# Optimization experiments

Hardware: AMD Instinct MI355X
Metric: run time of the kernel (lower is better)

Reference implementation:

```python
import jax, jax.numpy as jnp
import numpy as np

# Camera / renderer constants from the original forward():
#   renderer.eye = get_points_from_angles(2.732, 0, 90); Renderer defaults.
DIST, ELEV, AZIM = 2.732, 0.0, 90.0
VIEW_ANGLE = 30.0          # neural_renderer Renderer default viewing angle (deg)
S = 256                    # image_size (Renderer default)
SIGMA = 3e-3               # softness of the differentiable edge test
EPS = 1e-12


def _normalize(v):
    return v / (jnp.linalg.norm(v) + EPS)


def _project(vertices):
    """look_at + perspective projection -> 2D NDC coords. vertices: [B,N,3]."""
    e = jnp.deg2rad(jnp.float32(ELEV))
    a = jnp.deg2rad(jnp.float32(AZIM))
    eye = jnp.array([DIST * jnp.cos(e) * jnp.sin(a),
                     DIST * jnp.sin(e),
                     -DIST * jnp.cos(e) * jnp.cos(a)], dtype=jnp.float32)
    at = jnp.zeros(3, jnp.float32)
    up = jnp.array([0.0, 1.0, 0.0], jnp.float32)
    zax = _normalize(at - eye)
    xax = _normalize(jnp.cross(up, zax))
    yax = jnp.cross(zax, xax)
    R = jnp.stack([xax, yax, zax])                 # [3,3], rows = camera axes
    v_cam = (vertices - eye) @ R.T                 # [B,N,3]
    w = jnp.tan(jnp.deg2rad(jnp.float32(VIEW_ANGLE)))
    z = jnp.maximum(v_cam[..., 2], 1e-2)           # guard behind-camera verts
    return v_cam[..., :2] / (z[..., None] * w)     # [B,N,2]


def _rasterize_one(xy, faces):
    """Soft silhouette rasterization. xy: [N,2], faces: [F,3] -> [S,S]."""
    tri = xy[faces]                                # [F,3,2]
    ps = (jnp.arange(S, dtype=jnp.float32) + 0.5) / S * 2.0 - 1.0
    px = ps[None, :]                               # x along columns  [1,S]
    py = -ps[:, None]                              # y down rows      [S,1]
    v0, v1, v2 = tri[:, 0], tri[:, 1], tri[:, 2]   # each [F,2]
    # winding sign so "inside" => positive signed edge distance
    area = ((v1[:, 0] - v0[:, 0]) * (v2[:, 1] - v0[:, 1])
            - (v1[:, 1] - v0[:, 1]) * (v2[:, 0] - v0[:, 0]))
    s = jnp.where(area >= 0, 1.0, -1.0)            # [F]
    d = jnp.full((faces.shape[0], S, S), jnp.inf, jnp.float32)
    for a_, b_ in ((v0, v1), (v1, v2), (v2, v0)):
        e = b_ - a_                                # [F,2]
        c = (e[:, 0, None, None] * (py[None] - a_[:, 1, None, None])
             - e[:, 1, None, None] * (px[None] - a_[:, 0, None, None]))  # [F,S,S]
        d = jnp.minimum(d, s[:, None, None] * c /
                        (jnp.linalg.norm(e, axis=-1)[:, None, None] + EPS))
    prob = jax.nn.sigmoid(d / SIGMA)               # per-face coverage [F,S,S]
    return 1.0 - jnp.prod(1.0 - prob, axis=0)      # union over faces  [S,S]


def _render_silhouettes(vertices, faces):
    xy = _project(vertices)                        # [B,N,2]
    return jax.vmap(_rasterize_one)(xy, faces)     # [B,S,S]


def setup_inputs() -> dict:
    key = jax.random.key(0)
    k1, k2, k3 = jax.random.split(key, 3)
    N, F = 512, 1024
    # mesh vertices scaled so the object sits in front of the camera at d=2.732
    vertices = 0.3 * jax.random.normal(k1, (1, N, 3), jnp.float32)
    faces = jax.random.randint(k2, (1, F, 3), 0, N, jnp.int32)
    image_ref = jax.random.uniform(k3, (1, S, S), dtype=jnp.float32)
    return {"vertices": vertices, "image_ref": image_ref, "faces": faces}


def reference(vertices, image_ref, faces):
    sil = _render_silhouettes(vertices, faces)     # [B,S,S]
    return jnp.sum((sil - image_ref) ** 2)
```

## Files before the change

### kernel.cpp

```cpp
#include <hip/hip_runtime.h>
#include <math.h>

#define NV 512
#define NF 1024
#define IMS 256
#define TILE 8
#define TPD 32
#define NT 1024
#define CHUNK 256
constexpr float SIGMA = 0.003f;
constexpr float LOG2E = 1.4426950408889634f;
constexpr float PXSZ = 2.0f / (float)IMS;
constexpr float TILE_R = 3.5f * PXSZ;

#if __has_builtin(__builtin_amdgcn_exp2f)
#define EXP2(x) __builtin_amdgcn_exp2f(x)
#else
#define EXP2(x) exp2f(x)
#endif

__global__ __launch_bounds__(256) void prep_kernel(const float* __restrict__ verts,
                                                   const int* __restrict__ faces,
                                                   float* __restrict__ coef,
                                                   float* __restrict__ out) {
    int f = blockIdx.x * 256 + threadIdx.x;
    if (f == 0) out[0] = 0.0f;
    if (f >= NF) return;

    const float deg2rad = 0.017453292519943295f;
    float e = 0.0f * deg2rad, a = 90.0f * deg2rad;
    float ce = cosf(e), se = sinf(e), ca = cosf(a), sa = sinf(a);
    float ex = 2.732f * ce * sa, ey = 2.732f * se, ez = -2.732f * ce * ca;
    float zn = sqrtf(ex*ex + ey*ey + ez*ez) + 1e-12f;
    float zx = -ex/zn, zy = -ey/zn, zz = -ez/zn;
    float cx = 1.0f*zz, cyv = 0.0f, cz = -1.0f*zx;
    float xn = sqrtf(cx*cx + cyv*cyv + cz*cz) + 1e-12f;
    float xax_x = cx/xn, xax_y = cyv/xn, xax_z = cz/xn;
    float yx = zy*xax_z - zz*xax_y;
    float yy = zz*xax_x - zx*xax_z;
    float yz = zx*xax_y - zy*xax_x;
    float w = tanf(30.0f * deg2rad);

    int i0 = faces[f*3+0], i1 = faces[f*3+1], i2 = faces[f*3+2];
    float P[3][2];
    int idx[3] = {i0, i1, i2};
    #pragma unroll
    for (int k = 0; k < 3; ++k) {
        float vx = verts[idx[k]*3+0] - ex;
        float vy = verts[idx[k]*3+1] - ey;
        float vz = verts[idx[k]*3+2] - ez;
        float camx = xax_x*vx + xax_y*vy + xax_z*vz;
        float camy = yx*vx + yy*vy + yz*vz;
        float camz = zx*vx + zy*vy + zz*vz;
        float z = fmaxf(camz, 0.01f);
        float invzw = 1.0f / (z * w);
        P[k][0] = camx * invzw;
        P[k][1] = camy * invzw;
    }
    float area = (P[1][0]-P[0][0])*(P[2][1]-P[0][1]) - (P[1][1]-P[0][1])*(P[2][0]-P[0][0]);
    float s = (area >= 0.0f) ? 1.0f : -1.0f;
    float o[9];
    #pragma unroll
    for (int k = 0; k < 3; ++k) {
        float x0 = P[k][0],       y0 = P[k][1];
        float x1 = P[(k+1)%3][0], y1 = P[(k+1)%3][1];
        float ex_ = x1 - x0, ey_ = y1 - y0;
        float len = sqrtf(ex_*ex_ + ey_*ey_);
        float inv = s * (LOG2E / SIGMA) / (len + 1e-12f);
        o[k*3+0] = -ey_ * inv;
        o[k*3+1] =  ex_ * inv;
        o[k*3+2] = (ey_*x0 - ex_*y0) * inv;
    }
    float* dst = coef + f*12;
    #pragma unroll
    for (int k = 0; k < 9; ++k) dst[k] = o[k];
    dst[9] = dst[10] = dst[11] = 0.0f;
}

__global__ __launch_bounds__(256) void raster_kernel(const float* __restrict__ coef,
                                                     const float* __restrict__ img,
                                                     float* __restrict__ out) {
    __shared__ unsigned short slist[NF];
    __shared__ float4 scoef[CHUNK * 3];
    __shared__ float part[4][64];
    __shared__ int cnt, cov, done;
    int t = threadIdx.x;
    int tile = blockIdx.x;
    int ti = tile >> 5, tj = tile & 31;
    if (t == 0) { cnt = 0; cov = 0; done = 0; }
    __syncthreads();

    const float4* c4 = (const float4*)coef;
    float cxn = ((float)(tj * TILE) + 4.0f) * PXSZ - 1.0f;
    float cyn = -(((float)(ti * TILE) + 4.0f) * PXSZ - 1.0f);
    #pragma unroll
    for (int k = 0; k < NF / 256; ++k) {
        int f = t + 256 * k;
        float4 c0 = c4[f*3+0];
        float4 c1 = c4[f*3+1];
        float4 c2 = c4[f*3+2];
        float d0 = fmaf(c0.x, cxn, fmaf(c0.y, cyn, c0.z));
        float r0 = (fabsf(c0.x) + fabsf(c0.y)) * TILE_R;
        float d1 = fmaf(c0.w, cxn, fmaf(c1.x, cyn, c1.y));
        float r1 = (fabsf(c0.w) + fabsf(c1.x)) * TILE_R;
        float d2 = fmaf(c1.z, cxn, fmaf(c1.w, cyn, c2.x));
        float r2 = (fabsf(c1.z) + fabsf(c1.w)) * TILE_R;
        float t_hi = fminf(d0 + r0, fminf(d1 + r1, d2 + r2));
        float t_lo = fminf(d0 - r0, fminf(d1 - r1, d2 - r2));
        if (t_lo > 130.0f) atomicOr(&cov, 1);
        else if (t_hi > -26.0f) {
            int pos = atomicAdd(&cnt, 1);
            slist[pos] = (unsigned short)f;
        }
    }
    __syncthreads();

    int lane = t & 63, wave = t >> 6;
    int pi = ti * TILE + (lane >> 3);
    int pj = tj * TILE + (lane & 7);
    float px = ((float)pj + 0.5f) * PXSZ - 1.0f;
    float py = -(((float)pi + 0.5f) * PXSZ - 1.0f);
    float prod = 1.0f;
    int covered = cov;
    if (!covered) {
        int len = cnt;
        for (int base = 0; base < len; base += CHUNK) {
            int m = min(CHUNK, len - base);
            if (t < m) {
                int f = (int)slist[base + t];
                scoef[t*3+0] = c4[f*3+0];
                scoef[t*3+1] = c4[f*3+1];
                scoef[t*3+2] = c4[f*3+2];
            }
            __syncthreads();
            int it = 0;
            for (int j = wave; j < m; j += 4) {
                float4 c0 = scoef[j*3+0];
                float4 c1 = scoef[j*3+1];
                float4 c2 = scoef[j*3+2];
                float d0 = fmaf(c0.x, px, fmaf(c0.y, py, c0.z));
                float d1 = fmaf(c0.w, px, fmaf(c1.x, py, c1.y));
                float d2 = fmaf(c1.z, px, fmaf(c1.w, py, c2.x));
                float tm = fminf(d0, fminf(d1, d2));
                float ef = EXP2(tm);
                prod *= __builtin_amdgcn_rcpf(1.0f + ef);
                if ((++it & 7) == 0 && __ballot(prod > 0.0f) == 0ull) {
                    atomicOr(&done, 1);
                    break;
                }
            }
            __syncthreads();
            if (done) break;
        }
    }
    part[wave][lane] = prod;
    __syncthreads();

    if (wave == 0) {
        float pr = covered ? 0.0f
                 : part[0][lane] * part[1][lane] * part[2][lane] * part[3][lane];
        float sil = 1.0f - pr;
        float diff = sil - img[pi * IMS + pj];
        float v = diff * diff;
        #pragma unroll
        for (int o = 32; o > 0; o >>= 1) v += __shfl_down(v, o);
        if (lane == 0) atomicAdd(out, v);
    }
}

extern "C" void kernel_launch(void* const* d_in, const int* in_sizes, int n_in,
                              void* d_out, int out_size, void* d_ws, size_t ws_size,
                              hipStream_t stream) {
    const float* verts = (const float*)d_in[0];
    const float* img   = (const float*)d_in[1];
    const int*   faces = (const int*)d_in[2];
    float* out  = (float*)d_out;
    float* coef = (float*)d_ws;

    prep_kernel<<<4, 256, 0, stream>>>(verts, faces, coef, out);
    raster_kernel<<<NT, 256, 0, stream>>>(coef, img, out);
}
```

Baseline: 28.97 us.

## Fuse face setup into raster kernel, computing edge coefficients per block in LDS

Removes the separate prep kernel. Each of the 1024 tile blocks now projects all faces and keeps their edge coefficients in shared memory, and the output is zeroed with a memset. The raster loop reads coefficients straight from LDS through the culled list, with no chunked staging and no block-wide early-exit barrier. The cost is redundant projection work in every block and a 48KB LDS footprint that may lower occupancy. Early exit is now per wave only.

After: 34.72 us. 19.9% more time.

```diff
diff --git a/kernel.cpp b/kernel.cpp
--- a/kernel.cpp
+++ b/kernel.cpp
@@ -1,13 +1,10 @@
 #include <hip/hip_runtime.h>
 #include <math.h>
 
-#define NV 512
 #define NF 1024
 #define IMS 256
 #define TILE 8
-#define TPD 32
 #define NT 1024
-#define CHUNK 256
 constexpr float SIGMA = 0.003f;
 constexpr float LOG2E = 1.4426950408889634f;
 constexpr float PXSZ = 2.0f / (float)IMS;
@@ -19,13 +16,19 @@
 #define EXP2(x) exp2f(x)
 #endif
 
-__global__ __launch_bounds__(256) void prep_kernel(const float* __restrict__ verts,
-                                                   const int* __restrict__ faces,
-                                                   float* __restrict__ coef,
-                                                   float* __restrict__ out) {
-    int f = blockIdx.x * 256 + threadIdx.x;
-    if (f == 0) out[0] = 0.0f;
-    if (f >= NF) return;
+__global__ __launch_bounds__(256) void fused_kernel(const float* __restrict__ verts,
+                                                    const int* __restrict__ faces,
+                                                    const float* __restrict__ img,
+                                                    float* __restrict__ out) {
+    __shared__ float4 fc[NF * 3];
+    __shared__ unsigned short slist[NF];
+    __shared__ float part[4][64];
+    __shared__ int cnt, cov;
+    int t = threadIdx.x;
+    int tile = blockIdx.x;
+    int ti = tile >> 5, tj = tile & 31;
+    if (t == 0) { cnt = 0; cov = 0; }
+    __syncthreads();
 
     const float deg2rad = 0.017453292519943295f;
     float e = 0.0f * deg2rad, a = 90.0f * deg2rad;
@@ -41,70 +44,50 @@
     float yz = zx*xax_y - zy*xax_x;
     float w = tanf(30.0f * deg2rad);
 
-    int i0 = faces[f*3+0], i1 = faces[f*3+1], i2 = faces[f*3+2];
-    float P[3][2];
-    int idx[3] = {i0, i1, i2};
-    #pragma unroll
-    for (int k = 0; k < 3; ++k) {
-        float vx = verts[idx[k]*3+0] - ex;
-        float vy = verts[idx[k]*3+1] - ey;
-        float vz = verts[idx[k]*3+2] - ez;
-        float camx = xax_x*vx + xax_y*vy + xax_z*vz;
-        float camy = yx*vx + yy*vy + yz*vz;
-        float camz = zx*vx + zy*vy + zz*vz;
-        float z = fmaxf(camz, 0.01f);
-        float invzw = 1.0f / (z * w);
-        P[k][0] = camx * invzw;
-        P[k][1] = camy * invzw;
-    }
-    float area = (P[1][0]-P[0][0])*(P[2][1]-P[0][1]) - (P[1][1]-P[0][1])*(P[2][0]-P[0][0]);
-    float s = (area >= 0.0f) ? 1.0f : -1.0f;
-    float o[9];
-    #pragma unroll
-    for (int k = 0; k < 3; ++k) {
-        float x0 = P[k][0],       y0 = P[k][1];
-        float x1 = P[(k+1)%3][0], y1 = P[(k+1)%3][1];
-        float ex_ = x1 - x0, ey_ = y1 - y0;
-        float len = sqrtf(ex_*ex_ + ey_*ey_);
-        float inv = s * (LOG2E / SIGMA) / (len + 1e-12f);
-        o[k*3+0] = -ey_ * inv;
-        o[k*3+1] =  ex_ * inv;
-        o[k*3+2] = (ey_*x0 - ex_*y0) * inv;
-    }
-    float* dst = coef + f*12;
-    #pragma unroll
-    for (int k = 0; k < 9; ++k) dst[k] = o[k];
-    dst[9] = dst[10] = dst[11] = 0.0f;
-}
-
-__global__ __launch_bounds__(256) void raster_kernel(const float* __restrict__ coef,
-                                                     const float* __restrict__ img,
-                                                     float* __restrict__ out) {
-    __shared__ unsigned short slist[NF];
-    __shared__ float4 scoef[CHUNK * 3];
-    __shared__ float part[4][64];
-    __shared__ int cnt, cov, done;
-    int t = threadIdx.x;
-    int tile = blockIdx.x;
-    int ti = tile >> 5, tj = tile & 31;
-    if (t == 0) { cnt = 0; cov = 0; done = 0; }
-    __syncthreads();
-
-    const float4* c4 = (const float4*)coef;
     float cxn = ((float)(tj * TILE) + 4.0f) * PXSZ - 1.0f;
     float cyn = -(((float)(ti * TILE) + 4.0f) * PXSZ - 1.0f);
+
     #pragma unroll
     for (int k = 0; k < NF / 256; ++k) {
         int f = t + 256 * k;
-        float4 c0 = c4[f*3+0];
-        float4 c1 = c4[f*3+1];
-        float4 c2 = c4[f*3+2];
-        float d0 = fmaf(c0.x, cxn, fmaf(c0.y, cyn, c0.z));
-        float r0 = (fabsf(c0.x) + fabsf(c0.y)) * TILE_R;
-        float d1 = fmaf(c0.w, cxn, fmaf(c1.x, cyn, c1.y));
-        float r1 = (fabsf(c0.w) + fabsf(c1.x)) * TILE_R;
-        float d2 = fmaf(c1.z, cxn, fmaf(c1.w, cyn, c2.x));
-        float r2 = (fabsf(c1.z) + fabsf(c1.w)) * TILE_R;
+        int idx[3] = {faces[f*3+0], faces[f*3+1], faces[f*3+2]};
+        float P[3][2];
+        #pragma unroll
+        for (int kk = 0; kk < 3; ++kk) {
+            float vx = verts[idx[kk]*3+0] - ex;
+            float vy = verts[idx[kk]*3+1] - ey;
+            float vz = verts[idx[kk]*3+2] - ez;
+            float camx = xax_x*vx + xax_y*vy + xax_z*vz;
+            float camy = yx*vx + yy*vy + yz*vz;
+            float camz = zx*vx + zy*vy + zz*vz;
+            float z = fmaxf(camz, 0.01f);
+            float invzw = 1.0f / (z * w);
+            P[kk][0] = camx * invzw;
+            P[kk][1] = camy * invzw;
+        }
+        float area = (P[1][0]-P[0][0])*(P[2][1]-P[0][1]) - (P[1][1]-P[0][1])*(P[2][0]-P[0][0]);
+        float s = (area >= 0.0f) ? 1.0f : -1.0f;
+        float o[9];
+        #pragma unroll
+        for (int kk = 0; kk < 3; ++kk) {
+            float x0 = P[kk][0],       y0 = P[kk][1];
+            float x1 = P[(kk+1)%3][0], y1 = P[(kk+1)%3][1];
+            float ex_ = x1 - x0, ey_ = y1 - y0;
+            float len = sqrtf(ex_*ex_ + ey_*ey_);
+            float inv = s * (LOG2E / SIGMA) / (len + 1e-12f);
+            o[kk*3+0] = -ey_ * inv;
+            o[kk*3+1] =  ex_ * inv;
+            o[kk*3+2] = (ey_*x0 - ex_*y0) * inv;
+        }
+        fc[f*3+0] = make_float4(o[0], o[1], o[2], o[3]);
+        fc[f*3+1] = make_float4(o[4], o[5], o[6], o[7]);
+        fc[f*3+2] = make_float4(o[8], 0.0f, 0.0f, 0.0f);
+        float d0 = fmaf(o[0], cxn, fmaf(o[1], cyn, o[2]));
+        float r0 = (fabsf(o[0]) + fabsf(o[1])) * TILE_R;
+        float d1 = fmaf(o[3], cxn, fmaf(o[4], cyn, o[5]));
+        float r1 = (fabsf(o[3]) + fabsf(o[4])) * TILE_R;
+        float d2 = fmaf(o[6], cxn, fmaf(o[7], cyn, o[8]));
+        float r2 = (fabsf(o[6]) + fabsf(o[7])) * TILE_R;
         float t_hi = fminf(d0 + r0, fminf(d1 + r1, d2 + r2));
         float t_lo = fminf(d0 - r0, fminf(d1 - r1, d2 - r2));
         if (t_lo > 130.0f) atomicOr(&cov, 1);
@@ -124,33 +107,19 @@
     int covered = cov;
     if (!covered) {
         int len = cnt;
-        for (int base = 0; base < len; base += CHUNK) {
-            int m = min(CHUNK, len - base);
-            if (t < m) {
-                int f = (int)slist[base + t];
-                scoef[t*3+0] = c4[f*3+0];
-                scoef[t*3+1] = c4[f*3+1];
-                scoef[t*3+2] = c4[f*3+2];
-            }
-            __syncthreads();
-            int it = 0;
-            for (int j = wave; j < m; j += 4) {
-                float4 c0 = scoef[j*3+0];
-                float4 c1 = scoef[j*3+1];
-                float4 c2 = scoef[j*3+2];
-                float d0 = fmaf(c0.x, px, fmaf(c0.y, py, c0.z));
-                float d1 = fmaf(c0.w, px, fmaf(c1.x, py, c1.y));
-                float d2 = fmaf(c1.z, px, fmaf(c1.w, py, c2.x));
-                float tm = fminf(d0, fminf(d1, d2));
-                float ef = EXP2(tm);
-                prod *= __builtin_amdgcn_rcpf(1.0f + ef);
-                if ((++it & 7) == 0 && __ballot(prod > 0.0f) == 0ull) {
-                    atomicOr(&done, 1);
-                    break;
-                }
-            }
-            __syncthreads();
-            if (done) break;
+        int it = 0;
+        for (int j = wave; j < len; j += 4) {
+            int f = (int)slist[j];
+            float4 c0 = fc[f*3+0];
+            float4 c1 = fc[f*3+1];
+            float4 c2 = fc[f*3+2];
+            float d0 = fmaf(c0.x, px, fmaf(c0.y, py, c0.z));
+            float d1 = fmaf(c0.w, px, fmaf(c1.x, py, c1.y));
+            float d2 = fmaf(c1.z, px, fmaf(c1.w, py, c2.x));
+            float tm = fminf(d0, fminf(d1, d2));
+            float ef = EXP2(tm);
+            prod *= __builtin_amdgcn_rcpf(1.0f + ef);
+            if ((++it & 7) == 0 && __ballot(prod > 0.0f) == 0ull) break;
         }
     }
     part[wave][lane] = prod;
@@ -174,9 +143,8 @@
     const float* verts = (const float*)d_in[0];
     const float* img   = (const float*)d_in[1];
     const int*   faces = (const int*)d_in[2];
-    float* out  = (float*)d_out;
-    float* coef = (float*)d_ws;
+    float* out = (float*)d_out;
 
-    prep_kernel<<<4, 256, 0, stream>>>(verts, faces, coef, out);
-    raster_kernel<<<NT, 256, 0, stream>>>(coef, img, out);
+    hipMemsetAsync(out, 0, sizeof(float), stream);
+    fused_kernel<<<NT, 256, 0, stream>>>(verts, faces, img, out);
 }
```

## Double raster block size, early-exit culling, and deterministic last-block reduction

Applied to the files above, without the earlier changes.

Raster blocks grow to 512 threads (8 waves per 8x8 tile), so each wave handles fewer faces and coefficient chunks hold 512 faces. The culling loop now exits early once a face fully covers the tile. The shared done flag is replaced by a per-thread alive flag, so a wave that saturates stops shading while the other waves keep going. The final float atomicAdd is replaced by per-tile partial sums plus a last-block reduction driven by a counter. This adds a barrier on every culling iteration and a threadfence/counter step per block, and the larger blocks may lower occupancy.

Measured after the change: 39.42 us. 1.36x slower.

```diff
diff --git a/kernel.cpp b/kernel.cpp
--- a/kernel.cpp
+++ b/kernel.cpp
@@ -1,13 +1,11 @@
 #include <hip/hip_runtime.h>
 #include <math.h>
 
-#define NV 512
 #define NF 1024
 #define IMS 256
 #define TILE 8
-#define TPD 32
 #define NT 1024
-#define CHUNK 256
+#define BT 512
 constexpr float SIGMA = 0.003f;
 constexpr float LOG2E = 1.4426950408889634f;
 constexpr float PXSZ = 2.0f / (float)IMS;
@@ -22,9 +20,9 @@
 __global__ __launch_bounds__(256) void prep_kernel(const float* __restrict__ verts,
                                                    const int* __restrict__ faces,
                                                    float* __restrict__ coef,
-                                                   float* __restrict__ out) {
+                                                   int* __restrict__ counter) {
     int f = blockIdx.x * 256 + threadIdx.x;
-    if (f == 0) out[0] = 0.0f;
+    if (f == 0) *counter = 0;
     if (f >= NF) return;
 
     const float deg2rad = 0.017453292519943295f;
@@ -77,25 +75,28 @@
     dst[9] = dst[10] = dst[11] = 0.0f;
 }
 
-__global__ __launch_bounds__(256) void raster_kernel(const float* __restrict__ coef,
-                                                     const float* __restrict__ img,
-                                                     float* __restrict__ out) {
+__global__ __launch_bounds__(BT) void raster_kernel(const float* __restrict__ coef,
+                                                    const float* __restrict__ img,
+                                                    float* __restrict__ partials,
+                                                    int* __restrict__ counter,
+                                                    float* __restrict__ out) {
+    __shared__ float4 scoef[BT * 3];
     __shared__ unsigned short slist[NF];
-    __shared__ float4 scoef[CHUNK * 3];
-    __shared__ float part[4][64];
-    __shared__ int cnt, cov, done;
+    __shared__ float part[8][64];
+    __shared__ int cnt, cov, last;
     int t = threadIdx.x;
     int tile = blockIdx.x;
     int ti = tile >> 5, tj = tile & 31;
-    if (t == 0) { cnt = 0; cov = 0; done = 0; }
+    if (t == 0) { cnt = 0; cov = 0; }
     __syncthreads();
 
     const float4* c4 = (const float4*)coef;
     float cxn = ((float)(tj * TILE) + 4.0f) * PXSZ - 1.0f;
     float cyn = -(((float)(ti * TILE) + 4.0f) * PXSZ - 1.0f);
-    #pragma unroll
-    for (int k = 0; k < NF / 256; ++k) {
-        int f = t + 256 * k;
+
+    #pragma unroll
+    for (int k = 0; k < NF / BT; ++k) {
+        int f = t + BT * k;
         float4 c0 = c4[f*3+0];
         float4 c1 = c4[f*3+1];
         float4 c2 = c4[f*3+2];
@@ -112,8 +113,9 @@
             int pos = atomicAdd(&cnt, 1);
             slist[pos] = (unsigned short)f;
         }
-    }
-    __syncthreads();
+        __syncthreads();
+        if (cov) break;
+    }
 
     int lane = t & 63, wave = t >> 6;
     int pi = ti * TILE + (lane >> 3);
@@ -124,8 +126,9 @@
     int covered = cov;
     if (!covered) {
         int len = cnt;
-        for (int base = 0; base < len; base += CHUNK) {
-            int m = min(CHUNK, len - base);
+        bool alive = true;
+        for (int base = 0; base < len; base += BT) {
+            int m = min(BT, len - base);
             if (t < m) {
                 int f = (int)slist[base + t];
                 scoef[t*3+0] = c4[f*3+0];
@@ -133,38 +136,63 @@
                 scoef[t*3+2] = c4[f*3+2];
             }
             __syncthreads();
-            int it = 0;
-            for (int j = wave; j < m; j += 4) {
-                float4 c0 = scoef[j*3+0];
-                float4 c1 = scoef[j*3+1];
-                float4 c2 = scoef[j*3+2];
-                float d0 = fmaf(c0.x, px, fmaf(c0.y, py, c0.z));
-                float d1 = fmaf(c0.w, px, fmaf(c1.x, py, c1.y));
-                float d2 = fmaf(c1.z, px, fmaf(c1.w, py, c2.x));
-                float tm = fminf(d0, fminf(d1, d2));
-                float ef = EXP2(tm);
-                prod *= __builtin_amdgcn_rcpf(1.0f + ef);
-                if ((++it & 7) == 0 && __ballot(prod > 0.0f) == 0ull) {
-                    atomicOr(&done, 1);
-                    break;
+            if (alive) {
+                int it = 0;
+                for (int j = wave; j < m; j += 8) {
+                    float4 c0 = scoef[j*3+0];
+                    float4 c1 = scoef[j*3+1];
+                    float4 c2 = scoef[j*3+2];
+                    float d0 = fmaf(c0.x, px, fmaf(c0.y, py, c0.z));
+                    float d1 = fmaf(c0.w, px, fmaf(c1.x, py, c1.y));
+                    float d2 = fmaf(c1.z, px, fmaf(c1.w, py, c2.x));
+                    float tm = fminf(d0, fminf(d1, d2));
+                    float ef = EXP2(tm);
+                    prod *= __builtin_amdgcn_rcpf(1.0f + ef);
+                    if ((++it & 7) == 0 && __ballot(prod > 0.0f) == 0ull) { alive = false; break; }
                 }
             }
             __syncthreads();
-            if (done) break;
         }
     }
     part[wave][lane] = prod;
     __syncthreads();
 
-    if (wave == 0) {
+    float v = 0.0f;
+    if (t < 64) {
         float pr = covered ? 0.0f
-                 : part[0][lane] * part[1][lane] * part[2][lane] * part[3][lane];
+                 : part[0][t]*part[1][t]*part[2][t]*part[3][t]
+                 * part[4][t]*part[5][t]*part[6][t]*part[7][t];
         float sil = 1.0f - pr;
         float diff = sil - img[pi * IMS + pj];
-        float v = diff * diff;
+        v = diff * diff;
         #pragma unroll
         for (int o = 32; o > 0; o >>= 1) v += __shfl_down(v, o);
-        if (lane == 0) atomicAdd(out, v);
+    }
+    if (t == 0) {
+        __hip_atomic_store(&partials[tile], v, __ATOMIC_RELEASE, __HIP_MEMORY_SCOPE_AGENT);
+        __threadfence();
+        int old = atomicAdd(counter, 1);
+        last = (old == NT - 1) ? 1 : 0;
+    }
+    __syncthreads();
+
+    if (last) {
+        __threadfence();
+        float s = 0.0f;
+        #pragma unroll
+        for (int i = 0; i < NT / BT; ++i)
+            s += __hip_atomic_load(&partials[t + i * BT], __ATOMIC_RELAXED, __HIP_MEMORY_SCOPE_AGENT);
+        #pragma unroll
+        for (int o = 32; o > 0; o >>= 1) s += __shfl_down(s, o);
+        __shared__ float red[8];
+        if ((t & 63) == 0) red[t >> 6] = s;
+        __syncthreads();
+        if (t == 0) {
+            float tot = 0.0f;
+            #pragma unroll
+            for (int wv = 0; wv < 8; ++wv) tot += red[wv];
+            out[0] = tot;
+        }
     }
 }
 
@@ -174,9 +202,12 @@
     const float* verts = (const float*)d_in[0];
     const float* img   = (const float*)d_in[1];
     const int*   faces = (const int*)d_in[2];
-    float* out  = (float*)d_out;
-    float* coef = (float*)d_ws;
-
-    prep_kernel<<<4, 256, 0, stream>>>(verts, faces, coef, out);
-    raster_kernel<<<NT, 256, 0, stream>>>(coef, img, out);
+    float* out = (float*)d_out;
+    char* ws = (char*)d_ws;
+    float* coef     = (float*)ws;
+    float* partials = (float*)(ws + 49152);
+    int*   counter  = (int*)(ws + 49152 + 4096);
+
+    prep_kernel<<<4, 256, 0, stream>>>(verts, faces, coef, counter);
+    raster_kernel<<<NT, BT, 0, stream>>>(coef, img, partials, counter, out);
 }
```
